# Kernel tuning notes

Measured on AMD Instinct MI355X. Metric: run time of the kernel, lower is better.

The kernel has to match this reference:

```python
import jax, jax.numpy as jnp
import numpy as np

# ---- physical constants / lattice geometry (from GrapheneConfig) ----
EV_TO_J = 1.602176634e-19
A_LAT = 2.46e-10                      # lattice constant a [m]
T_EV, TP_EV, M_EV = 2.8, 0.1, 0.05    # t, t', mass in eV
A_CC = A_LAT / np.sqrt(3.0)           # carbon-carbon distance
SQ3 = np.sqrt(3.0)
# nearest-neighbor vectors deltas [3,2]
DELTAS = np.asarray(A_CC * np.array([[0.0, -1.0],
                                     [SQ3 / 2.0, 0.5],
                                     [-SQ3 / 2.0, 0.5]]), dtype=np.float32)
# next-nearest-neighbor vectors nnn [6,2]
NNN = np.asarray(A_LAT * np.array([[1.0, 0.0], [-1.0, 0.0],
                                   [0.5, SQ3 / 2.0], [-0.5, -SQ3 / 2.0],
                                   [0.5, -SQ3 / 2.0], [-0.5, SQ3 / 2.0]]), dtype=np.float32)
KMAX = 4.0 * np.pi / (3.0 * SQ3 * A_CC)  # Dirac-point |k| scale (analytic_K)

N_K = 4_194_304


def setup_inputs() -> dict:
    key = jax.random.key(0)
    # uniform k-points covering the Brillouin-zone scale [-kmax, kmax]^2
    k = (jax.random.uniform(key, (N_K, 2), dtype=jnp.float32) * 2.0 - 1.0) * KMAX
    return {"k": k}


def reference(k):
    """energies(k) for every k-point: eigvalsh of the 2x2 Hermitian
    h(k) = [[e+D, f], [conj(f), e-D]], computed in closed form
    (eigvalsh of a 2x2 Hermitian matrix == e -/+ sqrt(D^2 + |f|^2), ascending).
    Computed in eV internally for fp32 safety, scaled to Joules at the end
    (identical math: all terms share the common factor EV_TO_J)."""
    deltas = jnp.asarray(DELTAS)
    nnn = jnp.asarray(NNN)
    # f(k) = -t * sum_j exp(i deltas_j . k)   (split into re/im; real math)
    ph = k @ deltas.T                                  # [N,3]
    f_re = -T_EV * jnp.sum(jnp.cos(ph), axis=-1)       # [N]
    f_im = -T_EV * jnp.sum(jnp.sin(ph), axis=-1)
    # eps_diag(k) = -t' * sum_j cos(nnn_j . k)
    e = -TP_EV * jnp.sum(jnp.cos(k @ nnn.T), axis=-1)  # [N]
    r = jnp.sqrt(M_EV * M_EV + f_re * f_re + f_im * f_im)
    return jnp.stack([e - r, e + r], axis=-1) * EV_TO_J  # [N,2] ascending
```

## Files before the change

kernel.cpp:

```cpp
#include <hip/hip_runtime.h>
#include <math.h>


namespace {
constexpr double A_LAT_D = 2.46e-10;
constexpr float C_P  = (float)(A_LAT_D * 0.5);
constexpr float C_B  = (float)(A_LAT_D / (2.0 * 1.7320508075688772935));
constexpr float T_EV  = 2.8f;
constexpr float TP_EV = 0.1f;
constexpr float M_EV  = 0.05f;
constexpr float EVJ   = 1.602176634e-19f;
}

__device__ __forceinline__ void graphene_point(float kx, float ky,
                                               float& lo, float& hi) {
    float p = kx * C_P;
    float b = ky * C_B;
    float cp = __cosf(p);
    float cb = __cosf(b);
    float sb = __sinf(b);
    float cb2 = cb * cb;
    float c3b = cb * (4.0f * cb2 - 3.0f);
    float fre = -T_EV * (2.0f * cp * cb + 2.0f * cb2 - 1.0f);
    float fim = -T_EV * (2.0f * sb * (cp - cb));
    float e   = -2.0f * TP_EV * (2.0f * cp * cp - 1.0f + 2.0f * cp * c3b);
    float r   = sqrtf(M_EV * M_EV + fre * fre + fim * fim);
    lo = (e - r) * EVJ;
    hi = (e + r) * EVJ;
}

__global__ __launch_bounds__(256)
void graphene_kernel(const float4* __restrict__ k4, float4* __restrict__ out4, int n4) {
    int i = blockIdx.x * blockDim.x + threadIdx.x;
    if (i >= n4) return;
    float4 kv = k4[i];
    float4 o;
    graphene_point(kv.x, kv.y, o.x, o.y);
    graphene_point(kv.z, kv.w, o.z, o.w);
    out4[i] = o;
}

extern "C" void kernel_launch(void* const* d_in, const int* in_sizes, int n_in,
                              void* d_out, int out_size, void* d_ws, size_t ws_size,
                              hipStream_t stream) {
    const float4* k4 = (const float4*)d_in[0];
    float4* out4 = (float4*)d_out;
    int n_floats = in_sizes[0];
    int n4 = n_floats / 4;
    int block = 256;
    int grid = (n4 + block - 1) / block;
    graphene_kernel<<<grid, block, 0, stream>>>(k4, out4, n4);
}
```

Measured before the change: 16.26 us.

## Use grid-stride loop with 4-way unrolled loads and nontemporal stores

Replaces the one-thread-per-float4 launch with a fixed 2048-block grid-stride loop. Each thread issues four independent float4 loads before computing, and writes results with nontemporal stores. The aim is more memory-level parallelism per thread, less block launch overhead, and less cache pollution from output writes. The fixed grid size may underfill or serialize work depending on the CU count.

```diff
diff --git a/kernel.cpp b/kernel.cpp
--- a/kernel.cpp
+++ b/kernel.cpp
@@ -1,6 +1,8 @@
 #include <hip/hip_runtime.h>
 #include <math.h>
 
+
+typedef float f32x4 __attribute__((ext_vector_type(4)));
 
 namespace {
 constexpr double A_LAT_D = 2.46e-10;
@@ -29,25 +31,48 @@
     hi = (e + r) * EVJ;
 }
 
+__device__ __forceinline__ f32x4 graphene_pair(f32x4 kv) {
+    f32x4 o;
+    float ox, oy, oz, ow;
+    graphene_point(kv.x, kv.y, ox, oy);
+    graphene_point(kv.z, kv.w, oz, ow);
+    o.x = ox; o.y = oy; o.z = oz; o.w = ow;
+    return o;
+}
+
 __global__ __launch_bounds__(256)
-void graphene_kernel(const float4* __restrict__ k4, float4* __restrict__ out4, int n4) {
-    int i = blockIdx.x * blockDim.x + threadIdx.x;
-    if (i >= n4) return;
-    float4 kv = k4[i];
-    float4 o;
-    graphene_point(kv.x, kv.y, o.x, o.y);
-    graphene_point(kv.z, kv.w, o.z, o.w);
-    out4[i] = o;
+void graphene_kernel(const f32x4* __restrict__ k4, f32x4* __restrict__ out4, int n4) {
+    int tid    = blockIdx.x * blockDim.x + threadIdx.x;
+    int stride = gridDim.x * blockDim.x;
+
+    int i = tid;
+    for (; i + 3 * stride < n4; i += 4 * stride) {
+        f32x4 a = k4[i];
+        f32x4 b = k4[i + stride];
+        f32x4 c = k4[i + 2 * stride];
+        f32x4 d = k4[i + 3 * stride];
+        f32x4 oa = graphene_pair(a);
+        f32x4 ob = graphene_pair(b);
+        f32x4 oc = graphene_pair(c);
+        f32x4 od = graphene_pair(d);
+        __builtin_nontemporal_store(oa, &out4[i]);
+        __builtin_nontemporal_store(ob, &out4[i + stride]);
+        __builtin_nontemporal_store(oc, &out4[i + 2 * stride]);
+        __builtin_nontemporal_store(od, &out4[i + 3 * stride]);
+    }
+    for (; i < n4; i += stride) {
+        __builtin_nontemporal_store(graphene_pair(k4[i]), &out4[i]);
+    }
 }
 
 extern "C" void kernel_launch(void* const* d_in, const int* in_sizes, int n_in,
                               void* d_out, int out_size, void* d_ws, size_t ws_size,
                               hipStream_t stream) {
-    const float4* k4 = (const float4*)d_in[0];
-    float4* out4 = (float4*)d_out;
+    const f32x4* k4 = (const f32x4*)d_in[0];
+    f32x4* out4 = (f32x4*)d_out;
     int n_floats = in_sizes[0];
     int n4 = n_floats / 4;
     int block = 256;
-    int grid = (n4 + block - 1) / block;
+    int grid  = 2048;
     graphene_kernel<<<grid, block, 0, stream>>>(k4, out4, n4);
 }
```

New measurement: 15.00 us. 7.7% less time.
